# Kernel tuning notes

Measured on AMD Instinct MI355X. Metric: run time of the kernel, lower is better.

The kernel has to match this reference:

```python
import jax, jax.numpy as jnp
import numpy as np

NUM_HEADS = 16
DIM = 1024
HID = DIM // NUM_HEADS
B, S = 2, 2048
NEG_INF = -1e30


def setup_inputs() -> dict:
    key = jax.random.key(0)
    ks = jax.random.split(key, 8)
    def xavier(k, shape, fan_in, fan_out):
        limit = np.sqrt(6.0 / (fan_in + fan_out))
        return jax.random.uniform(k, shape, jnp.float32, -limit, limit)
    return {
        "q": jax.random.normal(ks[0], (B, S, DIM), jnp.float32),
        "k": jax.random.normal(ks[1], (B, S, DIM), jnp.float32),
        "v": jax.random.normal(ks[2], (B, S, DIM), jnp.float32),
        "Wq": xavier(ks[3], (1, NUM_HEADS, DIM, HID), DIM, HID),
        "Wk": xavier(ks[4], (1, NUM_HEADS, DIM, HID), DIM, HID),
        "Wv": xavier(ks[5], (1, NUM_HEADS, DIM, HID), DIM, HID),
        "Wo": xavier(ks[6], (1, DIM, DIM), DIM, DIM),
        "mask": jax.random.randint(ks[7], (B, S), 0, 2, jnp.int32),
    }


def reference(q, k, v, Wq, Wk, Wv, Wo, mask):
    b, s, d = q.shape
    norm = jnp.sqrt(jnp.asarray(HID, q.dtype))
    # per-head projections: [B,S,D] x [H,D,hd] -> [B,H,S,hd]
    qh = jnp.einsum('bsd,hde->bhse', q, Wq[0])
    kh = jnp.einsum('bsd,hde->bhse', k, Wk[0])
    vh = jnp.einsum('bsd,hde->bhse', v, Wv[0])
    scores = jnp.einsum('bhse,bhte->bhst', qh, kh) / norm  # [B,H,S,S]
    m = mask.astype(bool)
    # original fills masked rows AND cols with 0.0 (not -inf)
    pad = m[:, None, :, None] | m[:, None, None, :]
    scores = jnp.where(pad, 0.0, scores)
    causal = jnp.triu(jnp.ones((s, s), bool), 1)
    scores = jnp.where(causal, NEG_INF, scores)
    attn = jax.nn.softmax(scores, axis=-1)
    out = jnp.einsum('bhst,bhte->bhse', attn, vh)  # [B,H,S,hd]
    # faithful to original: raw view (memory reinterpretation), NO head transpose
    out = out.reshape(b, s, NUM_HEADS * HID)
    return out @ Wo[0]
```

## Files before the change

kernel.cpp:

```cpp
#include <hip/hip_runtime.h>
#include <hip/hip_bf16.h>

#define BB 2
#define SS 2048
#define DD 1024
#define HH 16
#define HD 64

typedef __attribute__((ext_vector_type(8))) short bf16x8;
typedef __attribute__((ext_vector_type(4))) float floatx4;

__device__ __forceinline__ short f2bf(float x) {
  __hip_bfloat16 h = __float2bfloat16(x);
  return __builtin_bit_cast(short, h);
}

__device__ __forceinline__ short f2bf_fast(float x) {
  unsigned u = __float_as_uint(x);
  return (short)((u + 0x7FFFu + ((u >> 16) & 1u)) >> 16);
}

__device__ __forceinline__ void load_lds16(const void* g, void* l) {
  __builtin_amdgcn_global_load_lds(
      (const __attribute__((address_space(1))) unsigned int*)g,
      (__attribute__((address_space(3))) unsigned int*)l, 16, 0, 0);
}

__device__ __forceinline__ float redsum16(float v) {
  v += __shfl_xor(v, 1, 64);
  v += __shfl_xor(v, 2, 64);
  v += __shfl_xor(v, 4, 64);
  v += __shfl_xor(v, 8, 64);
  return v;
}

__global__ __launch_bounds__(256) void prep(
    const float* __restrict__ q, const float* __restrict__ k,
    const float* __restrict__ v, const float* __restrict__ Wq,
    const float* __restrict__ Wk, const float* __restrict__ Wv,
    const float* __restrict__ Wo, short* __restrict__ qo,
    short* __restrict__ ko, short* __restrict__ vo, short* __restrict__ qT,
    short* __restrict__ kT, short* __restrict__ vT, short* __restrict__ WoT) {
  __shared__ short sT[64 * 72];
  const int blk = blockIdx.x;
  if (blk < 12288) {
    const int which = blk >> 12, x = blk & 4095;
    const float* src = which == 0 ? q : which == 1 ? k : v;
    short* dst       = which == 0 ? qo : which == 1 ? ko : vo;
    size_t i = ((size_t)x * 256 + threadIdx.x) * 4;
    float4 f = *(const float4*)(src + i);
    short4 s;
    s.x = f2bf(f.x); s.y = f2bf(f.y); s.z = f2bf(f.z); s.w = f2bf(f.w);
    *(short4*)(dst + i) = s;
    return;
  }
  const int t = threadIdx.x, r = t >> 2, c0 = (t & 3) * 16;
  const float* src;
  short* dst;
  if (blk < 13056) {
    const int b2 = blk - 12288, which = b2 >> 8, rr = b2 & 255;
    const int dtile = rr & 15, h = rr >> 4, d0 = dtile * 64;
    const float* W = which == 0 ? Wq : which == 1 ? Wk : Wv;
    short* WT      = which == 0 ? qT : which == 1 ? kT : vT;
    src = W + ((size_t)h * DD + d0 + r) * HD + c0;
    dst = WT + ((size_t)h * HD + r) * DD + d0 + c0;
  } else {
    const int b3 = blk - 13056;
    const int k0 = (b3 & 15) * 64, n0 = (b3 >> 4) * 64;
    src = Wo + (size_t)(k0 + r) * DD + n0 + c0;
    dst = WoT + (size_t)(n0 + r) * DD + k0 + c0;
  }
  const float4* s4 = (const float4*)src;
  float4 f0 = s4[0], f1 = s4[1], f2 = s4[2], f3 = s4[3];
  const float ff[16] = {f0.x, f0.y, f0.z, f0.w, f1.x, f1.y, f1.z, f1.w,
                        f2.x, f2.y, f2.z, f2.w, f3.x, f3.y, f3.z, f3.w};
#pragma unroll
  for (int j = 0; j < 16; ++j) sT[r * 72 + c0 + j] = f2bf(ff[j]);
  __syncthreads();
  alignas(16) short tmp[16];
#pragma unroll
  for (int j = 0; j < 16; ++j) tmp[j] = sT[(c0 + j) * 72 + r];
  *(int4*)(dst) = *(const int4*)(tmp);
  *(int4*)(dst + 8) = *(const int4*)(tmp + 8);
}

__global__ __launch_bounds__(256) void proj(
    const short* __restrict__ xq, const short* __restrict__ xk,
    const short* __restrict__ xv, const short* __restrict__ WqT,
    const short* __restrict__ WkT, const short* __restrict__ WvT,
    short* __restrict__ qh, short* __restrict__ kh, short* __restrict__ vhT) {
  __shared__ short sA[128 * 32];
  __shared__ short sB[128 * 32];
  __shared__ short sT2[128 * 136];
  const int xcd = blockIdx.x & 7, tt = blockIdx.x >> 3;
  const int which = tt >> 5;
  const int rest = tt & 31;
  const int j = ((xcd & 3) << 1) | (rest >> 4);
  const int i = ((xcd >> 2) << 4) | (rest & 15);
  const short* X  = which == 0 ? xq : which == 1 ? xk : xv;
  const short* WT = which == 0 ? WqT : which == 1 ? WkT : WvT;
  const int m0 = i * 128, n0 = j * 128;
  const int tid = threadIdx.x, wid = tid >> 6, lane = tid & 63;
  const int quad = lane >> 4, l16 = lane & 15;
  const int wr = wid >> 1, wc = wid & 1;

  floatx4 acc[4][4] = {};
  for (int k0 = 0; k0 < DD; k0 += 32) {
    __syncthreads();
#pragma unroll
    for (int ii = 0; ii < 2; ++ii) {
      const int c = wid * 2 + ii;
      const int ci = c * 64 + lane;
      load_lds16(X + (size_t)(m0 + (ci >> 2)) * DD + k0 + (ci & 3) * 8,
                 &sA[c * 512]);
      load_lds16(WT + (size_t)(n0 + (ci >> 2)) * DD + k0 + (ci & 3) * 8,
                 &sB[c * 512]);
    }
    __syncthreads();
    bf16x8 af[4], bfr[4];
#pragma unroll
    for (int mi = 0; mi < 4; ++mi)
      af[mi] = *(const bf16x8*)&sA[(wr * 64 + mi * 16 + l16) * 32 + quad * 8];
#pragma unroll
    for (int ni = 0; ni < 4; ++ni)
      bfr[ni] = *(const bf16x8*)&sB[(wc * 64 + ni * 16 + l16) * 32 + quad * 8];
#pragma unroll
    for (int mi = 0; mi < 4; ++mi)
#pragma unroll
      for (int ni = 0; ni < 4; ++ni)
        acc[mi][ni] = __builtin_amdgcn_mfma_f32_16x16x32_bf16(
            af[mi], bfr[ni], acc[mi][ni], 0, 0, 0);
  }
  if (which != 2) {
    short* dst = which == 0 ? qh : kh;
    const float scale = (which == 0) ? 0.125f : 1.0f;
#pragma unroll
    for (int mi = 0; mi < 4; ++mi)
#pragma unroll
      for (int ni = 0; ni < 4; ++ni)
#pragma unroll
        for (int r2 = 0; r2 < 4; ++r2) {
          const int m = m0 + wr * 64 + mi * 16 + quad * 4 + r2;
          const int n = n0 + wc * 64 + ni * 16 + l16;
          dst[(size_t)m * DD + n] = f2bf(acc[mi][ni][r2] * scale);
        }
  } else {
    __syncthreads();
#pragma unroll
    for (int mi = 0; mi < 4; ++mi)
#pragma unroll
      for (int ni = 0; ni < 4; ++ni)
#pragma unroll
        for (int r2 = 0; r2 < 4; ++r2) {
          const int ml = wr * 64 + mi * 16 + quad * 4 + r2;
          const int nl = wc * 64 + ni * 16 + l16;
          sT2[nl * 136 + ml] = f2bf(acc[mi][ni][r2]);
        }
    __syncthreads();
    const int b = m0 >> 11;
    const int row = tid >> 1, half = tid & 1;
    const int h = (n0 + row) >> 6, e = (n0 + row) & 63;
    short* dstp = vhT + ((size_t)(b * HH + h) * HD + e) * SS + (m0 & 2047) +
                  half * 64;
    const short* srcl = &sT2[row * 136 + half * 64];
#pragma unroll
    for (int jj = 0; jj < 8; ++jj)
      *(int4*)(dstp + jj * 8) = *(const int4*)(srcl + jj * 8);
  }
}

__global__ __launch_bounds__(256) void attn(
    const short* __restrict__ qh, const short* __restrict__ kh,
    const short* __restrict__ vhT, const int* __restrict__ mask,
    short* __restrict__ X) {
  __shared__ union {
    short sP[4][32 * 72];
    float red[2][40 * 64];
  } u;
  const int tid = threadIdx.x, wid = tid >> 6, lane = tid & 63;
  const int quad = lane >> 4, l16 = lane & 15;
  const int xcd = blockIdx.x & 7, slot = blockIdx.x >> 3;
  const int bh = (xcd << 2) | (slot & 3);
  const int strip = 63 - (slot >> 2);
  const int b = bh >> 4, h = bh & 15;
  const int row0 = strip * 32;

  const short* Q  = qh + (size_t)b * SS * DD + h * HD;
  const short* K  = kh + (size_t)b * SS * DD + h * HD;
  const short* Vt = vhT + (size_t)bh * HD * SS;
  const int* mk = mask + b * SS;

  bf16x8 aq[2][2];
#pragma unroll
  for (int mi = 0; mi < 2; ++mi)
#pragma unroll
    for (int ks = 0; ks < 2; ++ks)
      aq[mi][ks] = *(const bf16x8*)(Q + (size_t)(row0 + mi * 16 + l16) * DD +
                                    ks * 32 + quad * 8);
  bool mrowb[2][4];
#pragma unroll
  for (int mi = 0; mi < 2; ++mi)
#pragma unroll
    for (int r2 = 0; r2 < 4; ++r2)
      mrowb[mi][r2] = mk[row0 + mi * 16 + quad * 4 + r2] != 0;

  floatx4 o[2][4] = {};
  float lacc[2][4];
#pragma unroll
  for (int mi = 0; mi < 2; ++mi)
#pragma unroll
    for (int r2 = 0; r2 < 4; ++r2) lacc[mi][r2] = 0.f;

  const int ntiles = (row0 >> 6) + 1;
  for (int tb = wid; tb < ntiles; tb += 4) {
    const int t0 = tb * 64;
    bf16x8 bk[4][2], bv[4][2];
#pragma unroll
    for (int ni = 0; ni < 4; ++ni)
#pragma unroll
      for (int ks = 0; ks < 2; ++ks)
        bk[ni][ks] = *(const bf16x8*)(K + (size_t)(t0 + ni * 16 + l16) * DD +
                                      ks * 32 + quad * 8);
#pragma unroll
    for (int ei = 0; ei < 4; ++ei)
#pragma unroll
      for (int ks = 0; ks < 2; ++ks)
        bv[ei][ks] = *(const bf16x8*)(Vt + (size_t)(ei * 16 + l16) * SS + t0 +
                                      ks * 32 + quad * 8);
    bool mtb[4];
#pragma unroll
    for (int ni = 0; ni < 4; ++ni) mtb[ni] = mk[t0 + ni * 16 + l16] != 0;
    const bool diag = (tb == ntiles - 1);

#pragma unroll
    for (int mi = 0; mi < 2; ++mi) {
      floatx4 s[4] = {};
#pragma unroll
      for (int ks = 0; ks < 2; ++ks)
#pragma unroll
        for (int ni = 0; ni < 4; ++ni)
          s[ni] = __builtin_amdgcn_mfma_f32_16x16x32_bf16(
              aq[mi][ks], bk[ni][ks], s[ni], 0, 0, 0);
#pragma unroll
      for (int ni = 0; ni < 4; ++ni)
#pragma unroll
        for (int r2 = 0; r2 < 4; ++r2) {
          const float ev = __expf(s[ni][r2]);
          float p = mtb[ni] ? 1.f : ev;
          p = mrowb[mi][r2] ? 1.f : p;
          if (diag) {
            const int row = row0 + mi * 16 + quad * 4 + r2;
            const int col = t0 + ni * 16 + l16;
            if (col > row) p = 0.f;
          }
          lacc[mi][r2] += p;
          u.sP[wid][(mi * 16 + quad * 4 + r2) * 72 + ni * 16 + l16] =
              f2bf_fast(p);
        }
    }
#pragma unroll
    for (int ks = 0; ks < 2; ++ks) {
      bf16x8 ap[2];
#pragma unroll
      for (int mi = 0; mi < 2; ++mi)
        ap[mi] = *(const bf16x8*)&u.sP[wid][(mi * 16 + l16) * 72 + ks * 32 +
                                            quad * 8];
#pragma unroll
      for (int mi = 0; mi < 2; ++mi)
#pragma unroll
        for (int ei = 0; ei < 4; ++ei)
          o[mi][ei] = __builtin_amdgcn_mfma_f32_16x16x32_bf16(
              ap[mi], bv[ei][ks], o[mi][ei], 0, 0, 0);
    }
  }

  __syncthreads();
  auto dump = [&](float* dst) {
    int j = 0;
#pragma unroll
    for (int mi = 0; mi < 2; ++mi)
#pragma unroll
      for (int ei = 0; ei < 4; ++ei)
#pragma unroll
        for (int r2 = 0; r2 < 4; ++r2) dst[(j++) * 64 + lane] = o[mi][ei][r2];
#pragma unroll
    for (int mi = 0; mi < 2; ++mi)
#pragma unroll
      for (int r2 = 0; r2 < 4; ++r2) dst[(j++) * 64 + lane] = lacc[mi][r2];
  };
  auto accum = [&](const float* srcp) {
    int j = 0;
#pragma unroll
    for (int mi = 0; mi < 2; ++mi)
#pragma unroll
      for (int ei = 0; ei < 4; ++ei)
#pragma unroll
        for (int r2 = 0; r2 < 4; ++r2) o[mi][ei][r2] += srcp[(j++) * 64 + lane];
#pragma unroll
    for (int mi = 0; mi < 2; ++mi)
#pragma unroll
      for (int r2 = 0; r2 < 4; ++r2) lacc[mi][r2] += srcp[(j++) * 64 + lane];
  };
  if (wid == 1) dump(u.red[0]);
  if (wid == 3) dump(u.red[1]);
  __syncthreads();
  if (wid == 0) accum(u.red[0]);
  if (wid == 2) accum(u.red[1]);
  __syncthreads();
  if (wid == 2) dump(u.red[0]);
  __syncthreads();
  if (wid == 0) {
    accum(u.red[0]);
#pragma unroll
    for (int mi = 0; mi < 2; ++mi)
#pragma unroll
      for (int r2 = 0; r2 < 4; ++r2) {
        const float inv = 1.0f / redsum16(lacc[mi][r2]);
        const int srow = row0 + mi * 16 + quad * 4 + r2;
#pragma unroll
        for (int ei = 0; ei < 4; ++ei)
          X[((size_t)bh * SS + srow) * HD + ei * 16 + l16] =
              f2bf(o[mi][ei][r2] * inv);
      }
  }
}

__global__ __launch_bounds__(256) void oproj(const short* __restrict__ X,
                                             const short* __restrict__ WoT,
                                             float* __restrict__ out) {
  __shared__ short sA[128 * 32];
  __shared__ short sB[64 * 32];
  const int m0 = blockIdx.x * 128, n0 = blockIdx.y * 64;
  const int tid = threadIdx.x, wid = tid >> 6, lane = tid & 63;
  const int quad = lane >> 4, l16 = lane & 15;
  const int wr = wid >> 1, wc = wid & 1;

  floatx4 acc[4][2] = {};
  for (int k0 = 0; k0 < DD; k0 += 32) {
    __syncthreads();
#pragma unroll
    for (int i = 0; i < 2; ++i) {
      const int c = wid * 2 + i;
      const int ci = c * 64 + lane;
      load_lds16(X + (size_t)(m0 + (ci >> 2)) * DD + k0 + (ci & 3) * 8,
                 &sA[c * 512]);
    }
    {
      const int ci = wid * 64 + lane;
      load_lds16(WoT + (size_t)(n0 + (ci >> 2)) * DD + k0 + (ci & 3) * 8,
                 &sB[wid * 512]);
    }
    __syncthreads();
    bf16x8 af[4], bfr[2];
#pragma unroll
    for (int mi = 0; mi < 4; ++mi)
      af[mi] = *(const bf16x8*)&sA[(wr * 64 + mi * 16 + l16) * 32 + quad * 8];
#pragma unroll
    for (int ni = 0; ni < 2; ++ni)
      bfr[ni] = *(const bf16x8*)&sB[(wc * 32 + ni * 16 + l16) * 32 + quad * 8];
#pragma unroll
    for (int mi = 0; mi < 4; ++mi)
#pragma unroll
      for (int ni = 0; ni < 2; ++ni)
        acc[mi][ni] = __builtin_amdgcn_mfma_f32_16x16x32_bf16(
            af[mi], bfr[ni], acc[mi][ni], 0, 0, 0);
  }
#pragma unroll
  for (int mi = 0; mi < 4; ++mi)
#pragma unroll
    for (int ni = 0; ni < 2; ++ni)
#pragma unroll
      for (int r2 = 0; r2 < 4; ++r2)
        out[(size_t)(m0 + wr * 64 + mi * 16 + quad * 4 + r2) * DD + n0 +
            wc * 32 + ni * 16 + l16] = acc[mi][ni][r2];
}

extern "C" void kernel_launch(void* const* d_in, const int* in_sizes, int n_in,
                              void* d_out, int out_size, void* d_ws,
                              size_t ws_size, hipStream_t stream) {
  const float* q  = (const float*)d_in[0];
  const float* k  = (const float*)d_in[1];
  const float* v  = (const float*)d_in[2];
  const float* Wq = (const float*)d_in[3];
  const float* Wk = (const float*)d_in[4];
  const float* Wv = (const float*)d_in[5];
  const float* Wo = (const float*)d_in[6];
  const int* mask = (const int*)d_in[7];
  float* out = (float*)d_out;

  short* ws = (short*)d_ws;
  const size_t NIN = (size_t)BB * SS * DD;
  const size_t NWH = (size_t)HH * HD * DD;
  short* qb  = ws;
  short* kb  = ws + NIN;
  short* vb  = ws + 2 * NIN;
  short* WqT = ws + 3 * NIN;
  short* WkT = WqT + NWH;
  short* WvT = WkT + NWH;
  short* WoT = WvT + NWH;
  short* qhp = WoT + (size_t)DD * DD;
  short* khp = qhp + NIN;
  short* vhT = khp + NIN;
  short* Xp  = qb;

  prep<<<dim3(13312), 256, 0, stream>>>(q, k, v, Wq, Wk, Wv, Wo, qb, kb, vb,
                                        WqT, WkT, WvT, WoT);
  proj<<<dim3(768), 256, 0, stream>>>(qb, kb, vb, WqT, WkT, WvT, qhp, khp,
                                      vhT);
  attn<<<dim3(2048), 256, 0, stream>>>(qhp, khp, vhT, mask, Xp);
  oproj<<<dim3(32, 16), 256, 0, stream>>>(Xp, WoT, out);
}
```

Baseline: 239.9 us.

## Assign one query strip per wave, fold masks into projections, prefetch K

The padding mask moves into the Q/K projection epilogue: masked rows of qh and kh are zeroed, so their scores become 0, which reproduces the reference behaviour. Q is also pre-scaled by log2(e)/8 so attention can use a raw exp2. The attention kernel now gives each wave a whole 32-row strip instead of splitting key tiles across four waves. This removes the LDS cross-wave reduction and its barriers, and strips are paired so a block's waves have equal tile counts. K tiles are double-buffered in registers, and P is converted to bf16 with a packed cvt instruction. The grid shrinks to 512 blocks, which lowers total parallelism and may hurt latency hiding.

Result: slower. 271.4 us (+13.1%).

```diff
diff --git a/kernel.cpp b/kernel.cpp
--- a/kernel.cpp
+++ b/kernel.cpp
@@ -15,9 +15,10 @@
   return __builtin_bit_cast(short, h);
 }
 
-__device__ __forceinline__ short f2bf_fast(float x) {
-  unsigned u = __float_as_uint(x);
-  return (short)((u + 0x7FFFu + ((u >> 16) & 1u)) >> 16);
+__device__ __forceinline__ unsigned cvtpk_bf16(float lo, float hi) {
+  unsigned r;
+  asm("v_cvt_pk_bf16_f32 %0, %1, %2" : "=v"(r) : "v"(lo), "v"(hi));
+  return r;
 }
 
 __device__ __forceinline__ void load_lds16(const void* g, void* l) {
@@ -88,7 +89,8 @@
     const short* __restrict__ xq, const short* __restrict__ xk,
     const short* __restrict__ xv, const short* __restrict__ WqT,
     const short* __restrict__ WkT, const short* __restrict__ WvT,
-    short* __restrict__ qh, short* __restrict__ kh, short* __restrict__ vhT) {
+    const int* __restrict__ mask, short* __restrict__ qh,
+    short* __restrict__ kh, short* __restrict__ vhT) {
   __shared__ short sA[128 * 32];
   __shared__ short sB[128 * 32];
   __shared__ short sT2[128 * 136];
@@ -133,17 +135,19 @@
   }
   if (which != 2) {
     short* dst = which == 0 ? qh : kh;
-    const float scale = (which == 0) ? 0.125f : 1.0f;
-#pragma unroll
-    for (int mi = 0; mi < 4; ++mi)
-#pragma unroll
-      for (int ni = 0; ni < 4; ++ni)
-#pragma unroll
-        for (int r2 = 0; r2 < 4; ++r2) {
-          const int m = m0 + wr * 64 + mi * 16 + quad * 4 + r2;
+    const float scale = (which == 0) ? 0.18033688f : 1.0f;
+#pragma unroll
+    for (int mi = 0; mi < 4; ++mi)
+#pragma unroll
+      for (int r2 = 0; r2 < 4; ++r2) {
+        const int m = m0 + wr * 64 + mi * 16 + quad * 4 + r2;
+        const float rs = mask[m] ? 0.f : scale;
+#pragma unroll
+        for (int ni = 0; ni < 4; ++ni) {
           const int n = n0 + wc * 64 + ni * 16 + l16;
-          dst[(size_t)m * DD + n] = f2bf(acc[mi][ni][r2] * scale);
+          dst[(size_t)m * DD + n] = f2bf(acc[mi][ni][r2] * rs);
         }
+      }
   } else {
     __syncthreads();
 #pragma unroll
@@ -169,26 +173,26 @@
   }
 }
 
-__global__ __launch_bounds__(256) void attn(
+__global__ __launch_bounds__(256, 2) void attn(
     const short* __restrict__ qh, const short* __restrict__ kh,
-    const short* __restrict__ vhT, const int* __restrict__ mask,
-    short* __restrict__ X) {
-  __shared__ union {
-    short sP[4][32 * 72];
-    float red[2][40 * 64];
-  } u;
+    const short* __restrict__ vhT, short* __restrict__ X) {
+  __shared__ short sP[4][32 * 72];
   const int tid = threadIdx.x, wid = tid >> 6, lane = tid & 63;
   const int quad = lane >> 4, l16 = lane & 15;
-  const int xcd = blockIdx.x & 7, slot = blockIdx.x >> 3;
-  const int bh = (xcd << 2) | (slot & 3);
-  const int strip = 63 - (slot >> 2);
+  const int xcd = blockIdx.x & 7, rank = blockIdx.x >> 3;
+  const int task = rank * 4 + wid;
+  const int szc = task >> 3;
+  const int mm = task & 7;
+  const int bh = (xcd << 2) | (mm >> 1);
+  const int strip = 63 - 2 * szc - (mm & 1);
   const int b = bh >> 4, h = bh & 15;
   const int row0 = strip * 32;
+  const int ntiles = 32 - szc;
 
   const short* Q  = qh + (size_t)b * SS * DD + h * HD;
   const short* K  = kh + (size_t)b * SS * DD + h * HD;
   const short* Vt = vhT + (size_t)bh * HD * SS;
-  const int* mk = mask + b * SS;
+  short* sPw = sP[wid];
 
   bf16x8 aq[2][2];
 #pragma unroll
@@ -197,41 +201,37 @@
     for (int ks = 0; ks < 2; ++ks)
       aq[mi][ks] = *(const bf16x8*)(Q + (size_t)(row0 + mi * 16 + l16) * DD +
                                     ks * 32 + quad * 8);
-  bool mrowb[2][4];
-#pragma unroll
-  for (int mi = 0; mi < 2; ++mi)
-#pragma unroll
-    for (int r2 = 0; r2 < 4; ++r2)
-      mrowb[mi][r2] = mk[row0 + mi * 16 + quad * 4 + r2] != 0;
 
   floatx4 o[2][4] = {};
-  float lacc[2][4];
-#pragma unroll
-  for (int mi = 0; mi < 2; ++mi)
-#pragma unroll
-    for (int r2 = 0; r2 < 4; ++r2) lacc[mi][r2] = 0.f;
-
-  const int ntiles = (row0 >> 6) + 1;
-  for (int tb = wid; tb < ntiles; tb += 4) {
+  float lacc[2][4] = {};
+
+  bf16x8 bkA[4][2], bkB[4][2];
+#pragma unroll
+  for (int ni = 0; ni < 4; ++ni)
+#pragma unroll
+    for (int ks = 0; ks < 2; ++ks)
+      bkA[ni][ks] = *(const bf16x8*)(K + (size_t)(ni * 16 + l16) * DD +
+                                     ks * 32 + quad * 8);
+
+  auto step = [&](int tb, bf16x8 (&bkc)[4][2], bf16x8 (&bkn)[4][2]) {
     const int t0 = tb * 64;
-    bf16x8 bk[4][2], bv[4][2];
-#pragma unroll
-    for (int ni = 0; ni < 4; ++ni)
-#pragma unroll
-      for (int ks = 0; ks < 2; ++ks)
-        bk[ni][ks] = *(const bf16x8*)(K + (size_t)(t0 + ni * 16 + l16) * DD +
-                                      ks * 32 + quad * 8);
+    bf16x8 bv[4][2];
 #pragma unroll
     for (int ei = 0; ei < 4; ++ei)
 #pragma unroll
       for (int ks = 0; ks < 2; ++ks)
         bv[ei][ks] = *(const bf16x8*)(Vt + (size_t)(ei * 16 + l16) * SS + t0 +
                                       ks * 32 + quad * 8);
-    bool mtb[4];
-#pragma unroll
-    for (int ni = 0; ni < 4; ++ni) mtb[ni] = mk[t0 + ni * 16 + l16] != 0;
+    if (tb + 1 < ntiles) {
+#pragma unroll
+      for (int ni = 0; ni < 4; ++ni)
+#pragma unroll
+        for (int ks = 0; ks < 2; ++ks)
+          bkn[ni][ks] =
+              *(const bf16x8*)(K + (size_t)(t0 + 64 + ni * 16 + l16) * DD +
+                               ks * 32 + quad * 8);
+    }
     const bool diag = (tb == ntiles - 1);
-
 #pragma unroll
     for (int mi = 0; mi < 2; ++mi) {
       floatx4 s[4] = {};
@@ -240,22 +240,25 @@
 #pragma unroll
         for (int ni = 0; ni < 4; ++ni)
           s[ni] = __builtin_amdgcn_mfma_f32_16x16x32_bf16(
-              aq[mi][ks], bk[ni][ks], s[ni], 0, 0, 0);
+              aq[mi][ks], bkc[ni][ks], s[ni], 0, 0, 0);
 #pragma unroll
       for (int ni = 0; ni < 4; ++ni)
 #pragma unroll
-        for (int r2 = 0; r2 < 4; ++r2) {
-          const float ev = __expf(s[ni][r2]);
-          float p = mtb[ni] ? 1.f : ev;
-          p = mrowb[mi][r2] ? 1.f : p;
+        for (int r2p = 0; r2p < 2; ++r2p) {
+          float p0 = __builtin_amdgcn_exp2f(s[ni][2 * r2p]);
+          float p1 = __builtin_amdgcn_exp2f(s[ni][2 * r2p + 1]);
           if (diag) {
-            const int row = row0 + mi * 16 + quad * 4 + r2;
+            const int row = row0 + mi * 16 + quad * 4 + 2 * r2p;
             const int col = t0 + ni * 16 + l16;
-            if (col > row) p = 0.f;
+            if (col > row) p0 = 0.f;
+            if (col > row + 1) p1 = 0.f;
           }
-          lacc[mi][r2] += p;
-          u.sP[wid][(mi * 16 + quad * 4 + r2) * 72 + ni * 16 + l16] =
-              f2bf_fast(p);
+          lacc[mi][2 * r2p] += p0;
+          lacc[mi][2 * r2p + 1] += p1;
+          const unsigned pk = cvtpk_bf16(p0, p1);
+          short* wp = &sPw[(mi * 16 + quad * 4 + 2 * r2p) * 72 + ni * 16 + l16];
+          wp[0] = (short)pk;
+          wp[72] = (short)(pk >> 16);
         }
     }
 #pragma unroll
@@ -263,8 +266,8 @@
       bf16x8 ap[2];
 #pragma unroll
       for (int mi = 0; mi < 2; ++mi)
-        ap[mi] = *(const bf16x8*)&u.sP[wid][(mi * 16 + l16) * 72 + ks * 32 +
-                                            quad * 8];
+        ap[mi] = *(const bf16x8*)&sPw[(mi * 16 + l16) * 72 + ks * 32 +
+                                      quad * 8];
 #pragma unroll
       for (int mi = 0; mi < 2; ++mi)
 #pragma unroll
@@ -272,57 +275,27 @@
           o[mi][ei] = __builtin_amdgcn_mfma_f32_16x16x32_bf16(
               ap[mi], bv[ei][ks], o[mi][ei], 0, 0, 0);
     }
-  }
-
-  __syncthreads();
-  auto dump = [&](float* dst) {
-    int j = 0;
-#pragma unroll
-    for (int mi = 0; mi < 2; ++mi)
+  };
+
+  int tb = 0;
+  for (;;) {
+    step(tb, bkA, bkB);
+    if (++tb >= ntiles) break;
+    step(tb, bkB, bkA);
+    if (++tb >= ntiles) break;
+  }
+
+#pragma unroll
+  for (int mi = 0; mi < 2; ++mi)
+#pragma unroll
+    for (int r2 = 0; r2 < 4; ++r2) {
+      const float inv = 1.0f / redsum16(lacc[mi][r2]);
+      const int srow = row0 + mi * 16 + quad * 4 + r2;
 #pragma unroll
       for (int ei = 0; ei < 4; ++ei)
-#pragma unroll
-        for (int r2 = 0; r2 < 4; ++r2) dst[(j++) * 64 + lane] = o[mi][ei][r2];
-#pragma unroll
-    for (int mi = 0; mi < 2; ++mi)
-#pragma unroll
-      for (int r2 = 0; r2 < 4; ++r2) dst[(j++) * 64 + lane] = lacc[mi][r2];
-  };
-  auto accum = [&](const float* srcp) {
-    int j = 0;
-#pragma unroll
-    for (int mi = 0; mi < 2; ++mi)
-#pragma unroll
-      for (int ei = 0; ei < 4; ++ei)
-#pragma unroll
-        for (int r2 = 0; r2 < 4; ++r2) o[mi][ei][r2] += srcp[(j++) * 64 + lane];
-#pragma unroll
-    for (int mi = 0; mi < 2; ++mi)
-#pragma unroll
-      for (int r2 = 0; r2 < 4; ++r2) lacc[mi][r2] += srcp[(j++) * 64 + lane];
-  };
-  if (wid == 1) dump(u.red[0]);
-  if (wid == 3) dump(u.red[1]);
-  __syncthreads();
-  if (wid == 0) accum(u.red[0]);
-  if (wid == 2) accum(u.red[1]);
-  __syncthreads();
-  if (wid == 2) dump(u.red[0]);
-  __syncthreads();
-  if (wid == 0) {
-    accum(u.red[0]);
-#pragma unroll
-    for (int mi = 0; mi < 2; ++mi)
-#pragma unroll
-      for (int r2 = 0; r2 < 4; ++r2) {
-        const float inv = 1.0f / redsum16(lacc[mi][r2]);
-        const int srow = row0 + mi * 16 + quad * 4 + r2;
-#pragma unroll
-        for (int ei = 0; ei < 4; ++ei)
-          X[((size_t)bh * SS + srow) * HD + ei * 16 + l16] =
-              f2bf(o[mi][ei][r2] * inv);
-      }
-  }
+        X[((size_t)bh * SS + srow) * HD + ei * 16 + l16] =
+            f2bf(o[mi][ei][r2] * inv);
+    }
 }
 
 __global__ __launch_bounds__(256) void oproj(const short* __restrict__ X,
@@ -405,8 +378,8 @@
 
   prep<<<dim3(13312), 256, 0, stream>>>(q, k, v, Wq, Wk, Wv, Wo, qb, kb, vb,
                                         WqT, WkT, WvT, WoT);
-  proj<<<dim3(768), 256, 0, stream>>>(qb, kb, vb, WqT, WkT, WvT, qhp, khp,
-                                      vhT);
-  attn<<<dim3(2048), 256, 0, stream>>>(qhp, khp, vhT, mask, Xp);
+  proj<<<dim3(768), 256, 0, stream>>>(qb, kb, vb, WqT, WkT, WvT, mask, qhp,
+                                      khp, vhT);
+  attn<<<dim3(512), 256, 0, stream>>>(qhp, khp, vhT, Xp);
   oproj<<<dim3(32, 16), 256, 0, stream>>>(Xp, WoT, out);
 }
```
